# Kernel optimization log

Measured on AMD Instinct MI355X. Metric: run time of the kernel, lower is better.

The kernel has to match this reference:

```python
import jax, jax.numpy as jnp
import numpy as np

N = 20000      # nodes
E = 320000     # edges (before self-loops)
IN = 256       # in_channels
HID = 64       # hidden_channels
HEADS = 4      # num_heads
OUT = 64       # out_channels
NEG_SLOPE = 0.2  # GATConv default leaky-relu slope


def setup_inputs() -> dict:
    key = jax.random.key(0)
    ks = jax.random.split(key, 12)
    s = 0.1
    x = jax.random.normal(ks[0], (N, IN), dtype=jnp.float32)
    edge_index = jax.random.randint(ks[1], (2, E), 0, N, dtype=jnp.int64)
    # Layer 1: IN -> HID per head, HEADS heads, concat
    W1 = jax.random.normal(ks[2], (IN, HEADS * HID), dtype=jnp.float32) * s
    a1_src = jax.random.normal(ks[3], (HEADS, HID), dtype=jnp.float32) * s
    a1_dst = jax.random.normal(ks[4], (HEADS, HID), dtype=jnp.float32) * s
    b1 = jnp.zeros((HEADS * HID,), dtype=jnp.float32)
    # Layer 2: HEADS*HID -> OUT, 1 head, no concat
    W2 = jax.random.normal(ks[5], (HEADS * HID, OUT), dtype=jnp.float32) * s
    a2_src = jax.random.normal(ks[6], (1, OUT), dtype=jnp.float32) * s
    a2_dst = jax.random.normal(ks[7], (1, OUT), dtype=jnp.float32) * s
    b2 = jnp.zeros((OUT,), dtype=jnp.float32)
    return {"x": x, "edge_index": edge_index,
            "W1": W1, "a1_src": a1_src, "a1_dst": a1_dst, "b1": b1,
            "W2": W2, "a2_src": a2_src, "a2_dst": a2_dst, "b2": b2}


def _gat_layer(x, src, dst, W, a_src, a_dst, bias, heads, out_c, concat):
    n = x.shape[0]
    h = (x @ W).reshape(n, heads, out_c)                    # [N,H,C]
    e_src = jnp.einsum('nhc,hc->nh', h, a_src)              # [N,H]
    e_dst = jnp.einsum('nhc,hc->nh', h, a_dst)              # [N,H]
    logits = jax.nn.leaky_relu(e_src[src] + e_dst[dst], NEG_SLOPE)  # [E',H]
    # segment softmax over incoming edges of each dst node
    m = jax.ops.segment_max(logits, dst, num_segments=n)    # [N,H]
    p = jnp.exp(logits - m[dst])                            # [E',H]
    z = jax.ops.segment_sum(p, dst, num_segments=n)         # [N,H]
    alpha = p / z[dst]                                      # [E',H]
    out = jax.ops.segment_sum(h[src] * alpha[:, :, None], dst, num_segments=n)
    out = out.reshape(n, heads * out_c) if concat else out.mean(axis=1)
    return out + bias


def reference(x, edge_index, W1, a1_src, a1_dst, b1, W2, a2_src, a2_dst, b2):
    # PyG GATConv adds self-loops by default
    loop = jnp.arange(N, dtype=edge_index.dtype)
    src = jnp.concatenate([edge_index[0], loop])
    dst = jnp.concatenate([edge_index[1], loop])
    h = _gat_layer(x, src, dst, W1, a1_src, a1_dst, b1, HEADS, HID, True)
    h = jax.nn.elu(h)
    # F.dropout defaults training=False -> identity in eval reference
    out = _gat_layer(h, src, dst, W2, a2_src, a2_dst, b2, 1, OUT, False)
    return out
```

## Files before the change

kernel.cpp:

```cpp
#include <hip/hip_runtime.h>
#include <math.h>

#define NEG 0.2f
#define CSTRIDE 64

typedef __attribute__((ext_vector_type(8))) short bf16x8;
typedef __attribute__((ext_vector_type(4))) float f32x4;
typedef unsigned int u32;

__device__ inline float bf2f(unsigned short u) {
    union { unsigned int i; float f; } v; v.i = ((unsigned int)u) << 16; return v.f;
}
__device__ inline unsigned short f2bf(float f) {
    union { float f; unsigned int i; } v; v.f = f;
    unsigned int r = v.i + 0x7FFF + ((v.i >> 16) & 1);
    return (unsigned short)(r >> 16);
}
__device__ inline void unpack8(uint4 hv, float* o) {
    o[0] = bf2f((unsigned short)(hv.x & 0xffffu));
    o[1] = bf2f((unsigned short)(hv.x >> 16));
    o[2] = bf2f((unsigned short)(hv.y & 0xffffu));
    o[3] = bf2f((unsigned short)(hv.y >> 16));
    o[4] = bf2f((unsigned short)(hv.z & 0xffffu));
    o[5] = bf2f((unsigned short)(hv.z >> 16));
    o[6] = bf2f((unsigned short)(hv.w & 0xffffu));
    o[7] = bf2f((unsigned short)(hv.w >> 16));
}
__device__ inline void load_lds16(const unsigned short* g, unsigned short* l) {
    __builtin_amdgcn_global_load_lds((const __attribute__((address_space(1))) u32*)g,
                                     (__attribute__((address_space(3))) u32*)l, 16, 0, 0);
}

__device__ void gemm1_block(int bm, int bn, unsigned short* As, unsigned short* Bs,
                            const unsigned short* __restrict__ A,
                            const unsigned short* __restrict__ Bt,
                            unsigned short* __restrict__ C,
                            const float* __restrict__ a1s, const float* __restrict__ a1d,
                            float* __restrict__ es, float* __restrict__ ed, int M) {
    const int tid = threadIdx.x;
    const int wave = tid >> 6, lane = tid & 63;
    const int wm = (wave >> 1) * 64, wn = (wave & 1) * 64;
    const int lm = lane & 15, kq = lane >> 4;
    const int rA = lane >> 2, cA = (lane & 3) * 8;

    int grA[2], grB[2];
#pragma unroll
    for (int i = 0; i < 2; ++i) {
        int c = wave * 2 + i;
        int gr = bm + c * 16 + rA;
        if (gr >= M) gr = M - 1;
        grA[i] = gr;
        grB[i] = bn + c * 16 + rA;
    }

    auto stage = [&](int t, int b) {
        const int k0 = t * 32;
        const int ka = (k0 < 512) ? k0 : k0 - 512;
#pragma unroll
        for (int i = 0; i < 2; ++i) {
            int c = wave * 2 + i;
            load_lds16(A + (size_t)grA[i] * 512 + ka + cA, As + b * 4096 + c * 512);
            load_lds16(Bt + (size_t)grB[i] * 768 + k0 + cA, Bs + b * 4096 + c * 512);
        }
    };

    f32x4 acc[4][4] = {};
    stage(0, 0);
    stage(1, 1);
    int buf = 0;
    for (int t = 0; t < 24; ++t) {
        if (t < 22) {
            int nb = buf + 2;
            if (nb >= 3) nb -= 3;
            stage(t + 2, nb);
            asm volatile("s_waitcnt vmcnt(8)" ::: "memory");
        } else if (t == 22) {
            asm volatile("s_waitcnt vmcnt(4)" ::: "memory");
        } else {
            asm volatile("s_waitcnt vmcnt(0)" ::: "memory");
        }
        __builtin_amdgcn_s_barrier();
        __builtin_amdgcn_sched_barrier(0);
        bf16x8 af[4], bfr[4];
#pragma unroll
        for (int f = 0; f < 4; ++f) af[f] = *(const bf16x8*)(As + buf * 4096 + (wm + f * 16 + lm) * 32 + kq * 8);
#pragma unroll
        for (int f = 0; f < 4; ++f) bfr[f] = *(const bf16x8*)(Bs + buf * 4096 + (wn + f * 16 + lm) * 32 + kq * 8);
#pragma unroll
        for (int fr = 0; fr < 4; ++fr)
#pragma unroll
            for (int fc = 0; fc < 4; ++fc)
                acc[fr][fc] = __builtin_amdgcn_mfma_f32_16x16x32_bf16(af[fr], bfr[fc], acc[fr][fc], 0, 0, 0);
        __builtin_amdgcn_s_barrier();
        __builtin_amdgcn_sched_barrier(0);
        buf = (buf + 1 == 3) ? 0 : buf + 1;
    }
    const int head = (bn + wn) >> 6;
    float asv[4], adv[4];
#pragma unroll
    for (int fc = 0; fc < 4; ++fc) {
        int ch = fc * 16 + lm;
        asv[fc] = a1s[head * 64 + ch];
        adv[fc] = a1d[head * 64 + ch];
    }
#pragma unroll
    for (int fr = 0; fr < 4; ++fr)
#pragma unroll
        for (int i = 0; i < 4; ++i) {
            int row = bm + wm + fr * 16 + kq * 4 + i;
            float se = 0.f, de = 0.f;
#pragma unroll
            for (int fc = 0; fc < 4; ++fc) {
                float c = acc[fr][fc][i];
                se = fmaf(asv[fc], c, se);
                de = fmaf(adv[fc], c, de);
            }
#pragma unroll
            for (int off = 1; off < 16; off <<= 1) {
                se += __shfl_xor(se, off, 64);
                de += __shfl_xor(de, off, 64);
            }
            if (row < M) {
                if (lm == 0) { es[row * 4 + head] = se; ed[row * 4 + head] = de; }
#pragma unroll
                for (int fc = 0; fc < 4; ++fc)
                    C[(size_t)row * 256 + bn + wn + fc * 16 + lm] = f2bf(acc[fr][fc][i]);
            }
        }
}

__global__ __launch_bounds__(256) void pre(const float* __restrict__ x,
                                           const float* __restrict__ W1,
                                           const float* __restrict__ W2,
                                           unsigned short* __restrict__ xs,
                                           unsigned short* __restrict__ Wt1,
                                           unsigned short* __restrict__ Wt2,
                                           int* __restrict__ cnt,
                                           int xb, int wb, int N) {
    int b = blockIdx.x, tid = threadIdx.x;
    if (b < xb) {
        int i = b * 256 + tid;
        if (i >= N * 64) return;
        int e0 = i * 4;
        int node = e0 >> 8, c = e0 & 255;
        float4 f = *(const float4*)(x + e0);
        unsigned short h0 = f2bf(f.x), h1 = f2bf(f.y), h2 = f2bf(f.z), h3 = f2bf(f.w);
        uint2 hi, lo;
        hi.x = (u32)h0 | ((u32)h1 << 16);
        hi.y = (u32)h2 | ((u32)h3 << 16);
        lo.x = (u32)f2bf(f.x - bf2f(h0)) | ((u32)f2bf(f.y - bf2f(h1)) << 16);
        lo.y = (u32)f2bf(f.z - bf2f(h2)) | ((u32)f2bf(f.w - bf2f(h3)) << 16);
        *(uint2*)(xs + (size_t)node * 512 + c) = hi;
        *(uint2*)(xs + (size_t)node * 512 + 256 + c) = lo;
    } else if (b < xb + wb) {
        int i = (b - xb) * 256 + tid;
        const float* W;
        unsigned short* Wt;
        int outc;
        if (i < 256 * 768) { W = W1; Wt = Wt1; outc = 256; }
        else {
            i -= 256 * 768;
            if (i >= 64 * 768) return;
            W = W2; Wt = Wt2; outc = 64;
        }
        int n = i / 768, k = i % 768;
        int ksrc = (k < 256) ? k : (k < 512 ? k - 256 : k - 512);
        float f = W[(size_t)ksrc * outc + n];
        unsigned short h = f2bf(f);
        if (k >= 512) h = f2bf(f - bf2f(h));
        Wt[i] = h;
    } else {
        int i = (b - xb - wb) * 256 + tid;
        if (i < N) cnt[i] = 0;
    }
}

__global__ __launch_bounds__(256) void fused_g1fill(
    int gcnt,
    const unsigned short* __restrict__ A, const unsigned short* __restrict__ Bt,
    unsigned short* __restrict__ C,
    const float* __restrict__ a1s, const float* __restrict__ a1d,
    float* __restrict__ es, float* __restrict__ ed, int M,
    const int* __restrict__ ei, int E,
    int* __restrict__ cnt, int* __restrict__ csr) {
    __shared__ int uni[12288];
    if ((int)blockIdx.x < gcnt) {
        int gid = blockIdx.x;
        unsigned short* sm = (unsigned short*)uni;
        gemm1_block((gid >> 1) * 128, (gid & 1) * 128, sm, sm + 12288,
                    A, Bt, C, a1s, a1d, es, ed, M);
    } else {
        int e = (blockIdx.x - gcnt) * 256 + threadIdx.x;
        if (e < E + M) {
            int s, d;
            if (e < E) { s = ei[e]; d = ei[E + e]; }
            else       { s = d = e - E; }
            int c = atomicAdd(&cnt[d], 1);
            if (c < CSTRIDE) csr[(size_t)d * CSTRIDE + c] = s;
        }
    }
}

__global__ __launch_bounds__(256) void gemm2_scores(const unsigned short* __restrict__ A,
                                                    const unsigned short* __restrict__ Bt,
                                                    unsigned short* __restrict__ C,
                                                    const float* __restrict__ a2s,
                                                    const float* __restrict__ a2d,
                                                    float* __restrict__ es,
                                                    float* __restrict__ ed, int M) {
    __shared__ unsigned short As[3][128 * 32];
    __shared__ unsigned short Bs[3][64 * 32];
    const int tid = threadIdx.x;
    const int bm = blockIdx.x * 128;
    const int wave = tid >> 6, lane = tid & 63;
    const int wm = wave * 32;
    const int lm = lane & 15, kq = lane >> 4;
    const int rA = lane >> 2, cA = (lane & 3) * 8;

    int grA[2], grB;
#pragma unroll
    for (int i = 0; i < 2; ++i) {
        int c = wave * 2 + i;
        int gr = bm + c * 16 + rA;
        if (gr >= M) gr = M - 1;
        grA[i] = gr;
    }
    grB = wave * 16 + rA;

    auto stage = [&](int t, int b) {
        const int k0 = t * 32;
        const int ka = (k0 < 512) ? k0 : k0 - 512;
#pragma unroll
        for (int i = 0; i < 2; ++i) {
            int c = wave * 2 + i;
            load_lds16(A + (size_t)grA[i] * 512 + ka + cA, &As[b][c * 512]);
        }
        load_lds16(Bt + (size_t)grB * 768 + k0 + cA, &Bs[b][wave * 512]);
    };

    f32x4 acc[2][4] = {};
    stage(0, 0);
    stage(1, 1);
    int buf = 0;
    for (int t = 0; t < 24; ++t) {
        if (t < 22) {
            int nb = buf + 2;
            if (nb >= 3) nb -= 3;
            stage(t + 2, nb);
            asm volatile("s_waitcnt vmcnt(6)" ::: "memory");
        } else if (t == 22) {
            asm volatile("s_waitcnt vmcnt(3)" ::: "memory");
        } else {
            asm volatile("s_waitcnt vmcnt(0)" ::: "memory");
        }
        __builtin_amdgcn_s_barrier();
        __builtin_amdgcn_sched_barrier(0);
        bf16x8 af[2], bfr[4];
#pragma unroll
        for (int f = 0; f < 2; ++f) af[f] = *(const bf16x8*)(&As[buf][(wm + f * 16 + lm) * 32 + kq * 8]);
#pragma unroll
        for (int f = 0; f < 4; ++f) bfr[f] = *(const bf16x8*)(&Bs[buf][(f * 16 + lm) * 32 + kq * 8]);
#pragma unroll
        for (int fr = 0; fr < 2; ++fr)
#pragma unroll
            for (int fc = 0; fc < 4; ++fc)
                acc[fr][fc] = __builtin_amdgcn_mfma_f32_16x16x32_bf16(af[fr], bfr[fc], acc[fr][fc], 0, 0, 0);
        __builtin_amdgcn_s_barrier();
        __builtin_amdgcn_sched_barrier(0);
        buf = (buf + 1 == 3) ? 0 : buf + 1;
    }
    float asv[4], adv[4];
#pragma unroll
    for (int fc = 0; fc < 4; ++fc) {
        int ch = fc * 16 + lm;
        asv[fc] = a2s[ch];
        adv[fc] = a2d[ch];
    }
#pragma unroll
    for (int fr = 0; fr < 2; ++fr)
#pragma unroll
        for (int i = 0; i < 4; ++i) {
            int row = bm + wm + fr * 16 + kq * 4 + i;
            float se = 0.f, de = 0.f;
#pragma unroll
            for (int fc = 0; fc < 4; ++fc) {
                float c = acc[fr][fc][i];
                se = fmaf(asv[fc], c, se);
                de = fmaf(adv[fc], c, de);
            }
#pragma unroll
            for (int off = 1; off < 16; off <<= 1) {
                se += __shfl_xor(se, off, 64);
                de += __shfl_xor(de, off, 64);
            }
            if (row < M) {
                if (lm == 0) { es[row] = se; ed[row] = de; }
#pragma unroll
                for (int fc = 0; fc < 4; ++fc)
                    C[(size_t)row * 64 + fc * 16 + lm] = f2bf(acc[fr][fc][i]);
            }
        }
}

__global__ __launch_bounds__(256) void agg1(const unsigned short* __restrict__ h,
                                            const int* __restrict__ csr,
                                            const int* __restrict__ cnt,
                                            const float* __restrict__ es,
                                            const float* __restrict__ ed,
                                            const float* __restrict__ b1,
                                            unsigned short* __restrict__ outs, int n) {
    int node = blockIdx.x * 8 + (threadIdx.x >> 5);
    int g = threadIdx.x & 31;
    if (node >= n) return;
    int hh = g >> 3;
    int cb = g * 8;
    float edst = ed[node * 4 + hh];
    int j0 = node * CSTRIDE;
    int c0 = cnt[node];
    int j1 = j0 + (c0 < CSTRIDE ? c0 : CSTRIDE);
    float z0 = 0.f, z1 = 0.f, z2 = 0.f, z3 = 0.f;
    float a0[8] = {}, a1a[8] = {}, a2a[8] = {}, a3a[8] = {};
    int j = j0;
    for (; j + 4 <= j1; j += 4) {
        int s0 = csr[j], s1 = csr[j + 1], s2 = csr[j + 2], s3 = csr[j + 3];
        uint4 v0 = *(const uint4*)(h + (size_t)s0 * 256 + cb);
        uint4 v1 = *(const uint4*)(h + (size_t)s1 * 256 + cb);
        uint4 v2 = *(const uint4*)(h + (size_t)s2 * 256 + cb);
        uint4 v3 = *(const uint4*)(h + (size_t)s3 * 256 + cb);
        float l0 = es[s0 * 4 + hh] + edst;
        float l1 = es[s1 * 4 + hh] + edst;
        float l2 = es[s2 * 4 + hh] + edst;
        float l3 = es[s3 * 4 + hh] + edst;
        l0 = (l0 > 0.f) ? l0 : NEG * l0;
        l1 = (l1 > 0.f) ? l1 : NEG * l1;
        l2 = (l2 > 0.f) ? l2 : NEG * l2;
        l3 = (l3 > 0.f) ? l3 : NEG * l3;
        float p0 = __expf(l0), p1 = __expf(l1), p2 = __expf(l2), p3 = __expf(l3);
        z0 += p0; z1 += p1; z2 += p2; z3 += p3;
        float t[8];
        unpack8(v0, t);
#pragma unroll
        for (int c = 0; c < 8; ++c) a0[c] = fmaf(p0, t[c], a0[c]);
        unpack8(v1, t);
#pragma unroll
        for (int c = 0; c < 8; ++c) a1a[c] = fmaf(p1, t[c], a1a[c]);
        unpack8(v2, t);
#pragma unroll
        for (int c = 0; c < 8; ++c) a2a[c] = fmaf(p2, t[c], a2a[c]);
        unpack8(v3, t);
#pragma unroll
        for (int c = 0; c < 8; ++c) a3a[c] = fmaf(p3, t[c], a3a[c]);
    }
    for (; j < j1; ++j) {
        int s0 = csr[j];
        uint4 v0 = *(const uint4*)(h + (size_t)s0 * 256 + cb);
        float l0 = es[s0 * 4 + hh] + edst;
        l0 = (l0 > 0.f) ? l0 : NEG * l0;
        float p0 = __expf(l0);
        z0 += p0;
        float t[8];
        unpack8(v0, t);
#pragma unroll
        for (int c = 0; c < 8; ++c) a0[c] = fmaf(p0, t[c], a0[c]);
    }
    float z = (z0 + z1) + (z2 + z3);
    float inv = 1.f / z;
    float r[8];
    unsigned short qh[8], ql[8];
#pragma unroll
    for (int c = 0; c < 8; ++c) {
        r[c] = ((a0[c] + a1a[c]) + (a2a[c] + a3a[c])) * inv + b1[cb + c];
        r[c] = (r[c] > 0.f) ? r[c] : (__expf(r[c]) - 1.f);
        qh[c] = f2bf(r[c]);
        ql[c] = f2bf(r[c] - bf2f(qh[c]));
    }
    uint4 hiw, low;
    hiw.x = (u32)qh[0] | ((u32)qh[1] << 16);
    hiw.y = (u32)qh[2] | ((u32)qh[3] << 16);
    hiw.z = (u32)qh[4] | ((u32)qh[5] << 16);
    hiw.w = (u32)qh[6] | ((u32)qh[7] << 16);
    low.x = (u32)ql[0] | ((u32)ql[1] << 16);
    low.y = (u32)ql[2] | ((u32)ql[3] << 16);
    low.z = (u32)ql[4] | ((u32)ql[5] << 16);
    low.w = (u32)ql[6] | ((u32)ql[7] << 16);
    *(uint4*)(outs + (size_t)node * 512 + cb) = hiw;
    *(uint4*)(outs + (size_t)node * 512 + 256 + cb) = low;
}

__global__ __launch_bounds__(256) void agg2(const unsigned short* __restrict__ h,
                                            const int* __restrict__ csr,
                                            const int* __restrict__ cnt,
                                            const float* __restrict__ es,
                                            const float* __restrict__ ed,
                                            const float* __restrict__ b2,
                                            float* __restrict__ out, int n) {
    int node = blockIdx.x * 32 + (threadIdx.x >> 3);
    int g = threadIdx.x & 7;
    if (node >= n) return;
    int cb = g * 8;
    float edst = ed[node];
    int j0 = node * CSTRIDE;
    int c0 = cnt[node];
    int j1 = j0 + (c0 < CSTRIDE ? c0 : CSTRIDE);
    float z0 = 0.f, z1 = 0.f, z2 = 0.f, z3 = 0.f;
    float a0[8] = {}, a1a[8] = {}, a2a[8] = {}, a3a[8] = {};
    int j = j0;
    for (; j + 4 <= j1; j += 4) {
        int s0 = csr[j], s1 = csr[j + 1], s2 = csr[j + 2], s3 = csr[j + 3];
        uint4 v0 = *(const uint4*)(h + (size_t)s0 * 64 + cb);
        uint4 v1 = *(const uint4*)(h + (size_t)s1 * 64 + cb);
        uint4 v2 = *(const uint4*)(h + (size_t)s2 * 64 + cb);
        uint4 v3 = *(const uint4*)(h + (size_t)s3 * 64 + cb);
        float l0 = es[s0] + edst, l1 = es[s1] + edst, l2 = es[s2] + edst, l3 = es[s3] + edst;
        l0 = (l0 > 0.f) ? l0 : NEG * l0;
        l1 = (l1 > 0.f) ? l1 : NEG * l1;
        l2 = (l2 > 0.f) ? l2 : NEG * l2;
        l3 = (l3 > 0.f) ? l3 : NEG * l3;
        float p0 = __expf(l0), p1 = __expf(l1), p2 = __expf(l2), p3 = __expf(l3);
        z0 += p0; z1 += p1; z2 += p2; z3 += p3;
        float t[8];
        unpack8(v0, t);
#pragma unroll
        for (int c = 0; c < 8; ++c) a0[c] = fmaf(p0, t[c], a0[c]);
        unpack8(v1, t);
#pragma unroll
        for (int c = 0; c < 8; ++c) a1a[c] = fmaf(p1, t[c], a1a[c]);
        unpack8(v2, t);
#pragma unroll
        for (int c = 0; c < 8; ++c) a2a[c] = fmaf(p2, t[c], a2a[c]);
        unpack8(v3, t);
#pragma unroll
        for (int c = 0; c < 8; ++c) a3a[c] = fmaf(p3, t[c], a3a[c]);
    }
    for (; j < j1; ++j) {
        int s0 = csr[j];
        uint4 v0 = *(const uint4*)(h + (size_t)s0 * 64 + cb);
        float l0 = es[s0] + edst;
        l0 = (l0 > 0.f) ? l0 : NEG * l0;
        float p0 = __expf(l0);
        z0 += p0;
        float t[8];
        unpack8(v0, t);
#pragma unroll
        for (int c = 0; c < 8; ++c) a0[c] = fmaf(p0, t[c], a0[c]);
    }
    float z = (z0 + z1) + (z2 + z3);
    float inv = 1.f / z;
    float4 r0, r1;
    r0.x = ((a0[0] + a1a[0]) + (a2a[0] + a3a[0])) * inv + b2[cb + 0];
    r0.y = ((a0[1] + a1a[1]) + (a2a[1] + a3a[1])) * inv + b2[cb + 1];
    r0.z = ((a0[2] + a1a[2]) + (a2a[2] + a3a[2])) * inv + b2[cb + 2];
    r0.w = ((a0[3] + a1a[3]) + (a2a[3] + a3a[3])) * inv + b2[cb + 3];
    r1.x = ((a0[4] + a1a[4]) + (a2a[4] + a3a[4])) * inv + b2[cb + 4];
    r1.y = ((a0[5] + a1a[5]) + (a2a[5] + a3a[5])) * inv + b2[cb + 5];
    r1.z = ((a0[6] + a1a[6]) + (a2a[6] + a3a[6])) * inv + b2[cb + 6];
    r1.w = ((a0[7] + a1a[7]) + (a2a[7] + a3a[7])) * inv + b2[cb + 7];
    *(float4*)(out + (size_t)node * 64 + cb) = r0;
    *(float4*)(out + (size_t)node * 64 + cb + 4) = r1;
}

extern "C" void kernel_launch(void* const* d_in, const int* in_sizes, int n_in,
                              void* d_out, int out_size, void* d_ws, size_t ws_size,
                              hipStream_t stream) {
    const float* x   = (const float*)d_in[0];
    const int*   ei  = (const int*)d_in[1];
    const float* W1  = (const float*)d_in[2];
    const float* a1s = (const float*)d_in[3];
    const float* a1d = (const float*)d_in[4];
    const float* b1  = (const float*)d_in[5];
    const float* W2  = (const float*)d_in[6];
    const float* a2s = (const float*)d_in[7];
    const float* a2d = (const float*)d_in[8];
    const float* b2  = (const float*)d_in[9];
    float* out = (float*)d_out;

    const int N = in_sizes[0] / 256;
    const int E = in_sizes[1] / 2;

    char* p = (char*)d_ws;
    auto take = [&](size_t bytes) {
        char* r = p;
        p += (bytes + 255) & ~(size_t)255;
        return r;
    };
    int* cnt  = (int*)take((size_t)N * 4);
    int* csr  = (int*)take((size_t)N * CSTRIDE * 4);
    unsigned short* hstk = (unsigned short*)take((size_t)N * 512 * 2);
    unsigned short* Wt1  = (unsigned short*)take((size_t)256 * 768 * 2);
    unsigned short* Wt2  = (unsigned short*)take((size_t)64 * 768 * 2);
    unsigned short* h1   = (unsigned short*)take((size_t)N * 256 * 2);
    unsigned short* h2   = (unsigned short*)take((size_t)N * 64 * 2);
    float* es1 = (float*)take((size_t)N * 4 * 4);
    float* ed1 = (float*)take((size_t)N * 4 * 4);
    float* es2 = (float*)take((size_t)N * 4);
    float* ed2 = (float*)take((size_t)N * 4);

    int xb = (N * 64 + 255) / 256;
    int wb = (256 * 768 + 64 * 768 + 255) / 256;
    int zb = (N + 255) / 256;
    pre<<<xb + wb + zb, 256, 0, stream>>>(x, W1, W2, hstk, Wt1, Wt2, cnt, xb, wb, N);

    int GT = 2 * ((N + 127) / 128);
    int eb = (E + N + 255) / 256;
    fused_g1fill<<<GT + eb, 256, 0, stream>>>(GT, hstk, Wt1, h1, a1s, a1d, es1, ed1, N,
                                              ei, E, cnt, csr);

    agg1<<<(N + 7) / 8, 256, 0, stream>>>(h1, csr, cnt, es1, ed1, b1, hstk, N);

    gemm2_scores<<<(N + 127) / 128, 256, 0, stream>>>(hstk, Wt2, h2, a2s, a2d, es2, ed2, N);

    agg2<<<(N + 31) / 32, 256, 0, stream>>>(h2, csr, cnt, es2, ed2, b2, out, N);
}
```

Baseline: 168.9 us.

## Pre-scale scores by log2e, store byte offsets in CSR, halve gemm2 tile

The attention scores are pre-multiplied by log2(e) so the aggregation kernels can call exp2f directly, which removes a multiply per edge. The CSR now stores source indices pre-shifted into byte offsets (s<<9), so the gather addresses in agg1/agg2 become simple adds and shifts instead of 64-bit multiplies. The gemm2 tile drops from 128 to 64 rows so the launch uses more blocks and fills the GPU better. Because of the shift, the offsets overflow int32 once N exceeds about 4M, and the code ties the CSR layout to the exact row sizes of h1 and h2.

```diff
diff --git a/kernel.cpp b/kernel.cpp
--- a/kernel.cpp
+++ b/kernel.cpp
@@ -3,6 +3,7 @@
 
 #define NEG 0.2f
 #define CSTRIDE 64
+#define LOG2E 1.4426950408889634f
 
 typedef __attribute__((ext_vector_type(8))) short bf16x8;
 typedef __attribute__((ext_vector_type(4))) float f32x4;
@@ -121,7 +122,10 @@
                 de += __shfl_xor(de, off, 64);
             }
             if (row < M) {
-                if (lm == 0) { es[row * 4 + head] = se; ed[row * 4 + head] = de; }
+                if (lm == 0) {
+                    es[row * 4 + head] = se * LOG2E;
+                    ed[row * 4 + head] = de * LOG2E;
+                }
 #pragma unroll
                 for (int fc = 0; fc < 4; ++fc)
                     C[(size_t)row * 256 + bn + wn + fc * 16 + lm] = f2bf(acc[fr][fc][i]);
@@ -196,7 +200,7 @@
             if (e < E) { s = ei[e]; d = ei[E + e]; }
             else       { s = d = e - E; }
             int c = atomicAdd(&cnt[d], 1);
-            if (c < CSTRIDE) csr[(size_t)d * CSTRIDE + c] = s;
+            if (c < CSTRIDE) csr[(size_t)d * CSTRIDE + c] = s << 9;
         }
     }
 }
@@ -208,37 +212,27 @@
                                                     const float* __restrict__ a2d,
                                                     float* __restrict__ es,
                                                     float* __restrict__ ed, int M) {
-    __shared__ unsigned short As[3][128 * 32];
+    __shared__ unsigned short As[3][64 * 32];
     __shared__ unsigned short Bs[3][64 * 32];
     const int tid = threadIdx.x;
-    const int bm = blockIdx.x * 128;
+    const int bm = blockIdx.x * 64;
     const int wave = tid >> 6, lane = tid & 63;
-    const int wm = wave * 32;
+    const int wm = wave * 16;
     const int lm = lane & 15, kq = lane >> 4;
     const int rA = lane >> 2, cA = (lane & 3) * 8;
 
-    int grA[2], grB;
-#pragma unroll
-    for (int i = 0; i < 2; ++i) {
-        int c = wave * 2 + i;
-        int gr = bm + c * 16 + rA;
-        if (gr >= M) gr = M - 1;
-        grA[i] = gr;
-    }
-    grB = wave * 16 + rA;
+    int grA = bm + wave * 16 + rA;
+    if (grA >= M) grA = M - 1;
+    int grB = wave * 16 + rA;
 
     auto stage = [&](int t, int b) {
         const int k0 = t * 32;
         const int ka = (k0 < 512) ? k0 : k0 - 512;
-#pragma unroll
-        for (int i = 0; i < 2; ++i) {
-            int c = wave * 2 + i;
-            load_lds16(A + (size_t)grA[i] * 512 + ka + cA, &As[b][c * 512]);
-        }
+        load_lds16(A + (size_t)grA * 512 + ka + cA, &As[b][wave * 512]);
         load_lds16(Bt + (size_t)grB * 768 + k0 + cA, &Bs[b][wave * 512]);
     };
 
-    f32x4 acc[2][4] = {};
+    f32x4 acc[4] = {};
     stage(0, 0);
     stage(1, 1);
     int buf = 0;
@@ -247,24 +241,21 @@
             int nb = buf + 2;
             if (nb >= 3) nb -= 3;
             stage(t + 2, nb);
-            asm volatile("s_waitcnt vmcnt(6)" ::: "memory");
+            asm volatile("s_waitcnt vmcnt(4)" ::: "memory");
         } else if (t == 22) {
-            asm volatile("s_waitcnt vmcnt(3)" ::: "memory");
+            asm volatile("s_waitcnt vmcnt(2)" ::: "memory");
         } else {
             asm volatile("s_waitcnt vmcnt(0)" ::: "memory");
         }
         __builtin_amdgcn_s_barrier();
         __builtin_amdgcn_sched_barrier(0);
-        bf16x8 af[2], bfr[4];
-#pragma unroll
-        for (int f = 0; f < 2; ++f) af[f] = *(const bf16x8*)(&As[buf][(wm + f * 16 + lm) * 32 + kq * 8]);
+        bf16x8 af = *(const bf16x8*)(&As[buf][(wm + lm) * 32 + kq * 8]);
+        bf16x8 bfr[4];
 #pragma unroll
         for (int f = 0; f < 4; ++f) bfr[f] = *(const bf16x8*)(&Bs[buf][(f * 16 + lm) * 32 + kq * 8]);
 #pragma unroll
-        for (int fr = 0; fr < 2; ++fr)
-#pragma unroll
-            for (int fc = 0; fc < 4; ++fc)
-                acc[fr][fc] = __builtin_amdgcn_mfma_f32_16x16x32_bf16(af[fr], bfr[fc], acc[fr][fc], 0, 0, 0);
+        for (int fc = 0; fc < 4; ++fc)
+            acc[fc] = __builtin_amdgcn_mfma_f32_16x16x32_bf16(af, bfr[fc], acc[fc], 0, 0, 0);
         __builtin_amdgcn_s_barrier();
         __builtin_amdgcn_sched_barrier(0);
         buf = (buf + 1 == 3) ? 0 : buf + 1;
@@ -277,29 +268,30 @@
         adv[fc] = a2d[ch];
     }
 #pragma unroll
-    for (int fr = 0; fr < 2; ++fr)
-#pragma unroll
-        for (int i = 0; i < 4; ++i) {
-            int row = bm + wm + fr * 16 + kq * 4 + i;
-            float se = 0.f, de = 0.f;
-#pragma unroll
-            for (int fc = 0; fc < 4; ++fc) {
-                float c = acc[fr][fc][i];
-                se = fmaf(asv[fc], c, se);
-                de = fmaf(adv[fc], c, de);
+    for (int i = 0; i < 4; ++i) {
+        int row = bm + wm + kq * 4 + i;
+        float se = 0.f, de = 0.f;
+#pragma unroll
+        for (int fc = 0; fc < 4; ++fc) {
+            float c = acc[fc][i];
+            se = fmaf(asv[fc], c, se);
+            de = fmaf(adv[fc], c, de);
+        }
+#pragma unroll
+        for (int off = 1; off < 16; off <<= 1) {
+            se += __shfl_xor(se, off, 64);
+            de += __shfl_xor(de, off, 64);
+        }
+        if (row < M) {
+            if (lm == 0) {
+                es[row] = se * LOG2E;
+                ed[row] = de * LOG2E;
             }
 #pragma unroll
-            for (int off = 1; off < 16; off <<= 1) {
-                se += __shfl_xor(se, off, 64);
-                de += __shfl_xor(de, off, 64);
-            }
-            if (row < M) {
-                if (lm == 0) { es[row] = se; ed[row] = de; }
-#pragma unroll
-                for (int fc = 0; fc < 4; ++fc)
-                    C[(size_t)row * 64 + fc * 16 + lm] = f2bf(acc[fr][fc][i]);
-            }
-        }
+            for (int fc = 0; fc < 4; ++fc)
+                C[(size_t)row * 64 + fc * 16 + lm] = f2bf(acc[fc][i]);
+        }
+    }
 }
 
 __global__ __launch_bounds__(256) void agg1(const unsigned short* __restrict__ h,
@@ -314,6 +306,10 @@
     if (node >= n) return;
     int hh = g >> 3;
     int cb = g * 8;
+    int cb2 = cb * 2;
+    int hh4 = hh * 4;
+    const char* hb = (const char*)h;
+    const char* eb = (const char*)es;
     float edst = ed[node * 4 + hh];
     int j0 = node * CSTRIDE;
     int c0 = cnt[node];
@@ -322,20 +318,20 @@
     float a0[8] = {}, a1a[8] = {}, a2a[8] = {}, a3a[8] = {};
     int j = j0;
     for (; j + 4 <= j1; j += 4) {
-        int s0 = csr[j], s1 = csr[j + 1], s2 = csr[j + 2], s3 = csr[j + 3];
-        uint4 v0 = *(const uint4*)(h + (size_t)s0 * 256 + cb);
-        uint4 v1 = *(const uint4*)(h + (size_t)s1 * 256 + cb);
-        uint4 v2 = *(const uint4*)(h + (size_t)s2 * 256 + cb);
-        uint4 v3 = *(const uint4*)(h + (size_t)s3 * 256 + cb);
-        float l0 = es[s0 * 4 + hh] + edst;
-        float l1 = es[s1 * 4 + hh] + edst;
-        float l2 = es[s2 * 4 + hh] + edst;
-        float l3 = es[s3 * 4 + hh] + edst;
+        int o0 = csr[j], o1 = csr[j + 1], o2 = csr[j + 2], o3 = csr[j + 3];
+        uint4 v0 = *(const uint4*)(hb + o0 + cb2);
+        uint4 v1 = *(const uint4*)(hb + o1 + cb2);
+        uint4 v2 = *(const uint4*)(hb + o2 + cb2);
+        uint4 v3 = *(const uint4*)(hb + o3 + cb2);
+        float l0 = *(const float*)(eb + (o0 >> 5) + hh4) + edst;
+        float l1 = *(const float*)(eb + (o1 >> 5) + hh4) + edst;
+        float l2 = *(const float*)(eb + (o2 >> 5) + hh4) + edst;
+        float l3 = *(const float*)(eb + (o3 >> 5) + hh4) + edst;
         l0 = (l0 > 0.f) ? l0 : NEG * l0;
         l1 = (l1 > 0.f) ? l1 : NEG * l1;
         l2 = (l2 > 0.f) ? l2 : NEG * l2;
         l3 = (l3 > 0.f) ? l3 : NEG * l3;
-        float p0 = __expf(l0), p1 = __expf(l1), p2 = __expf(l2), p3 = __expf(l3);
+        float p0 = exp2f(l0), p1 = exp2f(l1), p2 = exp2f(l2), p3 = exp2f(l3);
         z0 += p0; z1 += p1; z2 += p2; z3 += p3;
         float t[8];
         unpack8(v0, t);
@@ -352,11 +348,11 @@
         for (int c = 0; c < 8; ++c) a3a[c] = fmaf(p3, t[c], a3a[c]);
     }
     for (; j < j1; ++j) {
-        int s0 = csr[j];
-        uint4 v0 = *(const uint4*)(h + (size_t)s0 * 256 + cb);
-        float l0 = es[s0 * 4 + hh] + edst;
+        int o0 = csr[j];
+        uint4 v0 = *(const uint4*)(hb + o0 + cb2);
+        float l0 = *(const float*)(eb + (o0 >> 5) + hh4) + edst;
         l0 = (l0 > 0.f) ? l0 : NEG * l0;
-        float p0 = __expf(l0);
+        float p0 = exp2f(l0);
         z0 += p0;
         float t[8];
         unpack8(v0, t);
@@ -398,6 +394,9 @@
     int g = threadIdx.x & 7;
     if (node >= n) return;
     int cb = g * 8;
+    int cb2 = cb * 2;
+    const char* hb = (const char*)h;
+    const char* eb = (const char*)es;
     float edst = ed[node];
     int j0 = node * CSTRIDE;
     int c0 = cnt[node];
@@ -406,17 +405,20 @@
     float a0[8] = {}, a1a[8] = {}, a2a[8] = {}, a3a[8] = {};
     int j = j0;
     for (; j + 4 <= j1; j += 4) {
-        int s0 = csr[j], s1 = csr[j + 1], s2 = csr[j + 2], s3 = csr[j + 3];
-        uint4 v0 = *(const uint4*)(h + (size_t)s0 * 64 + cb);
-        uint4 v1 = *(const uint4*)(h + (size_t)s1 * 64 + cb);
-        uint4 v2 = *(const uint4*)(h + (size_t)s2 * 64 + cb);
-        uint4 v3 = *(const uint4*)(h + (size_t)s3 * 64 + cb);
-        float l0 = es[s0] + edst, l1 = es[s1] + edst, l2 = es[s2] + edst, l3 = es[s3] + edst;
+        int o0 = csr[j], o1 = csr[j + 1], o2 = csr[j + 2], o3 = csr[j + 3];
+        uint4 v0 = *(const uint4*)(hb + (o0 >> 2) + cb2);
+        uint4 v1 = *(const uint4*)(hb + (o1 >> 2) + cb2);
+        uint4 v2 = *(const uint4*)(hb + (o2 >> 2) + cb2);
+        uint4 v3 = *(const uint4*)(hb + (o3 >> 2) + cb2);
+        float l0 = *(const float*)(eb + (o0 >> 7)) + edst;
+        float l1 = *(const float*)(eb + (o1 >> 7)) + edst;
+        float l2 = *(const float*)(eb + (o2 >> 7)) + edst;
+        float l3 = *(const float*)(eb + (o3 >> 7)) + edst;
         l0 = (l0 > 0.f) ? l0 : NEG * l0;
         l1 = (l1 > 0.f) ? l1 : NEG * l1;
         l2 = (l2 > 0.f) ? l2 : NEG * l2;
         l3 = (l3 > 0.f) ? l3 : NEG * l3;
-        float p0 = __expf(l0), p1 = __expf(l1), p2 = __expf(l2), p3 = __expf(l3);
+        float p0 = exp2f(l0), p1 = exp2f(l1), p2 = exp2f(l2), p3 = exp2f(l3);
         z0 += p0; z1 += p1; z2 += p2; z3 += p3;
         float t[8];
         unpack8(v0, t);
@@ -433,11 +435,11 @@
         for (int c = 0; c < 8; ++c) a3a[c] = fmaf(p3, t[c], a3a[c]);
     }
     for (; j < j1; ++j) {
-        int s0 = csr[j];
-        uint4 v0 = *(const uint4*)(h + (size_t)s0 * 64 + cb);
-        float l0 = es[s0] + edst;
+        int o0 = csr[j];
+        uint4 v0 = *(const uint4*)(hb + (o0 >> 2) + cb2);
+        float l0 = *(const float*)(eb + (o0 >> 7)) + edst;
         l0 = (l0 > 0.f) ? l0 : NEG * l0;
-        float p0 = __expf(l0);
+        float p0 = exp2f(l0);
         z0 += p0;
         float t[8];
         unpack8(v0, t);
@@ -507,7 +509,7 @@
 
     agg1<<<(N + 7) / 8, 256, 0, stream>>>(h1, csr, cnt, es1, ed1, b1, hstk, N);
 
-    gemm2_scores<<<(N + 127) / 128, 256, 0, stream>>>(hstk, Wt2, h2, a2s, a2d, es2, ed2, N);
+    gemm2_scores<<<(N + 63) / 64, 256, 0, stream>>>(hstk, Wt2, h2, a2s, a2d, es2, ed2, N);
 
     agg2<<<(N + 31) / 32, 256, 0, stream>>>(h2, csr, cnt, es2, ed2, b2, out, N);
 }
```

Measured after the change: 166.5 us. Within noise of the previous version (-1.4%).
